# Performance work log

Measured on AMD Instinct MI355X. Metric: run time of the kernel, lower is better.

## Reference

```python
import jax, jax.numpy as jnp
import numpy as np

NUM_EXPERTS = 8
TOP_K = 2
HIDDEN = 2048
INTER = 1024
B, S = 4, 1024


def setup_inputs() -> dict:
    key = jax.random.key(0)
    ks = jax.random.split(key, 5)
    sx = 1.0 / np.sqrt(HIDDEN)
    si = 1.0 / np.sqrt(INTER)
    return {
        "x": jax.random.normal(ks[0], (B, S, HIDDEN), dtype=jnp.float32),
        # router gate: Linear(hidden -> num_experts), weight stored [E, H] (torch convention)
        "gate_w": jax.random.normal(ks[1], (NUM_EXPERTS, HIDDEN), dtype=jnp.float32) * sx,
        # stacked expert weights: gate/up [E, I, H], down [E, H, I]
        "gate_proj_w": jax.random.normal(ks[2], (NUM_EXPERTS, INTER, HIDDEN), dtype=jnp.float32) * sx,
        "up_proj_w": jax.random.normal(ks[3], (NUM_EXPERTS, INTER, HIDDEN), dtype=jnp.float32) * sx,
        "down_proj_w": jax.random.normal(ks[4], (NUM_EXPERTS, HIDDEN, INTER), dtype=jnp.float32) * si,
    }


def _moe_forward(x, gate_w, gate_proj_w, up_proj_w, down_proj_w):
    Bx, Sx, H = x.shape
    T = Bx * Sx
    h = x.reshape(T, H)
    # --- routing (Qwen3: softmax in fp32, top-k, renormalize) ---
    router_logits = h @ gate_w.T                                   # [T, E]
    probs = jax.nn.softmax(router_logits.astype(jnp.float32), axis=-1)
    top_vals, top_idx = jax.lax.top_k(probs, TOP_K)                # [T, K]
    top_vals = top_vals / jnp.sum(top_vals, axis=-1, keepdims=True)  # norm_topk_prob
    # dense routing weights [T, E]: zero for unselected experts
    rw = jnp.zeros((T, NUM_EXPERTS), dtype=jnp.float32)
    rw = rw.at[jnp.arange(T)[:, None], top_idx].add(top_vals)
    rw = rw.astype(h.dtype)
    # --- SwiGLU experts, computed densely and masked by routing weights ---
    g = jnp.einsum('th,eih->tei', h, gate_proj_w)                  # [T, E, I]
    u = jnp.einsum('th,eih->tei', h, up_proj_w)                    # [T, E, I]
    a = jax.nn.silu(g) * u                                         # [T, E, I]
    out_e = jnp.einsum('tei,ehi->teh', a, down_proj_w)             # [T, E, H]
    out = jnp.einsum('te,teh->th', rw, out_e)                      # [T, H]
    return out.reshape(Bx, Sx, H)


def reference(x, gate_w, gate_proj_w, up_proj_w, down_proj_w):
    return _moe_forward(x, gate_w, gate_proj_w, up_proj_w, down_proj_w)
```

## Files before the change

kernel.cpp:

```cpp
#include <hip/hip_runtime.h>
#include <hip/hip_bf16.h>

#define NUM_EXPERTS 8
#define HIDDEN 2048
#define INTER 1024
#define T_TOKENS 4096

#define BK 32
#define GU_BM 64
#define GU_BN 128
#define DN_BM 64
#define DN_BN 128

typedef __attribute__((ext_vector_type(8))) short short8;
typedef __attribute__((ext_vector_type(4))) float f32x4;

__device__ __forceinline__ ushort f2bf(float f) {
    __hip_bfloat16 h = __float2bfloat16(f);
    return *reinterpret_cast<ushort*>(&h);
}

__device__ __forceinline__ void load_lds16(const void* g, void* lds) {
    __builtin_amdgcn_global_load_lds(
        (const __attribute__((address_space(1))) void*)g,
        (__attribute__((address_space(3))) void*)lds, 16, 0, 0);
}

__global__ __launch_bounds__(256) void cvt_bf16(const float* __restrict__ in,
                                                ushort* __restrict__ out, int n4) {
    int i = blockIdx.x * 256 + threadIdx.x;
    int stride = gridDim.x * 256;
    for (; i < n4; i += stride) {
        float4 v = reinterpret_cast<const float4*>(in)[i];
        ushort4 o;
        o.x = f2bf(v.x); o.y = f2bf(v.y); o.z = f2bf(v.z); o.w = f2bf(v.w);
        reinterpret_cast<ushort4*>(out)[i] = o;
    }
}

__global__ __launch_bounds__(64) void moe_router(const float* __restrict__ x,
                                                 const float* __restrict__ gw,
                                                 int* __restrict__ top_idx,
                                                 float* __restrict__ top_w,
                                                 int* __restrict__ counts) {
    int t = blockIdx.x;
    int lane = threadIdx.x;
    const float* xt = x + (size_t)t * HIDDEN;
    float acc[NUM_EXPERTS];
#pragma unroll
    for (int e = 0; e < NUM_EXPERTS; e++) acc[e] = 0.f;
    for (int h = lane; h < HIDDEN; h += 64) {
        float xv = xt[h];
#pragma unroll
        for (int e = 0; e < NUM_EXPERTS; e++)
            acc[e] = fmaf(xv, gw[e * HIDDEN + h], acc[e]);
    }
#pragma unroll
    for (int e = 0; e < NUM_EXPERTS; e++) {
#pragma unroll
        for (int off = 32; off > 0; off >>= 1)
            acc[e] += __shfl_xor(acc[e], off);
    }
    if (lane == 0) {
        int i1 = 0; float l1 = acc[0];
#pragma unroll
        for (int e = 1; e < NUM_EXPERTS; e++)
            if (acc[e] > l1) { l1 = acc[e]; i1 = e; }
        int i2 = -1; float l2 = -3.4e38f;
#pragma unroll
        for (int e = 0; e < NUM_EXPERTS; e++)
            if (e != i1 && acc[e] > l2) { l2 = acc[e]; i2 = e; }
        float w2 = __expf(l2 - l1);
        float denom = 1.f + w2;
        top_idx[t * 2 + 0] = i1;
        top_idx[t * 2 + 1] = i2;
        top_w[t * 2 + 0] = 1.f / denom;
        top_w[t * 2 + 1] = w2 / denom;
        atomicAdd(&counts[i1], 1);
        atomicAdd(&counts[i2], 1);
    }
}

__global__ void moe_offsets(const int* __restrict__ counts,
                            int* __restrict__ ebase, int* __restrict__ cursor) {
    if (threadIdx.x == 0 && blockIdx.x == 0) {
        int s = 0;
        for (int e = 0; e < NUM_EXPERTS; e++) {
            ebase[e] = s; cursor[e] = s; s += counts[e];
        }
    }
}

__global__ __launch_bounds__(256) void moe_scatter(const int* __restrict__ top_idx,
                                                   const float* __restrict__ top_w,
                                                   int* __restrict__ cursor,
                                                   int* __restrict__ slot_tok,
                                                   float* __restrict__ slot_w) {
    int t = blockIdx.x * 256 + threadIdx.x;
    if (t >= T_TOKENS) return;
#pragma unroll
    for (int k = 0; k < 2; k++) {
        int e = top_idx[t * 2 + k];
        int pos = atomicAdd(&cursor[e], 1);
        slot_tok[pos] = t;
        slot_w[pos] = top_w[t * 2 + k];
    }
}

__global__ __launch_bounds__(256, 3) void moe_gateup(const ushort* __restrict__ xb,
                                                     const ushort* __restrict__ wgb,
                                                     const ushort* __restrict__ wub,
                                                     const int* __restrict__ slot_tok,
                                                     const int* __restrict__ ebase,
                                                     const int* __restrict__ ecnt,
                                                     ushort* __restrict__ act) {
    __shared__ ushort ldsA[2][GU_BM * BK];
    __shared__ ushort ldsG[2][GU_BN * BK];
    __shared__ ushort ldsU[2][GU_BN * BK];

    const int e = blockIdx.z;
    const int bm = blockIdx.y;
    const int bn = blockIdx.x;
    const int cnt = ecnt[e];
    if (bm * GU_BM >= cnt) return;
    const int b0 = ebase[e];

    const int tid = threadIdx.x;
    const int lane = tid & 63;
    const int wid = tid >> 6;
    const int wr = wid >> 1, wc = wid & 1;

    const int r = tid >> 2, cs = tid & 3;
    const int scl = (cs ^ ((r >> 1) & 3)) * 8;
    const int ar = bm * GU_BM + r;
    const int tok = slot_tok[b0 + ((ar < cnt) ? ar : (cnt - 1))];
    const ushort* pA = xb + (size_t)tok * HIDDEN + scl;
    const size_t wrow0 = (size_t)e * INTER + (size_t)(bn * GU_BN + r);
    const ushort* pG0 = wgb + wrow0 * HIDDEN + scl;
    const ushort* pG1 = pG0 + (size_t)64 * HIDDEN;
    const ushort* pU0 = wub + wrow0 * HIDDEN + scl;
    const ushort* pU1 = pU0 + (size_t)64 * HIDDEN;

    const int fr = lane & 15;
    const int colsw = (((lane >> 4) ^ ((fr >> 1) & 3)) * 8);

    f32x4 accg[2][4] = {};
    f32x4 accu[2][4] = {};

#define GU_STAGE(buf, t)                                              \
    do {                                                              \
        const int _o = (t) * BK;                                      \
        load_lds16(pA + _o,  &ldsA[buf][tid * 8]);                    \
        load_lds16(pG0 + _o, &ldsG[buf][tid * 8]);                    \
        load_lds16(pG1 + _o, &ldsG[buf][2048 + tid * 8]);             \
        load_lds16(pU0 + _o, &ldsU[buf][tid * 8]);                    \
        load_lds16(pU1 + _o, &ldsU[buf][2048 + tid * 8]);             \
    } while (0)

    GU_STAGE(0, 0);
    __syncthreads();

    int cur = 0;
    const int NT = HIDDEN / BK;
    for (int t = 0; t < NT; ++t) {
        if (t + 1 < NT) GU_STAGE(cur ^ 1, t + 1);

        const ushort* LA = ldsA[cur];
        const ushort* LG = ldsG[cur];
        const ushort* LU = ldsU[cur];
        short8 a[2], bg[4], bu[4];
#pragma unroll
        for (int m = 0; m < 2; m++)
            a[m] = *(const short8*)(LA + (wr * 32 + m * 16 + fr) * BK + colsw);
#pragma unroll
        for (int n = 0; n < 4; n++) {
            bg[n] = *(const short8*)(LG + (wc * 64 + n * 16 + fr) * BK + colsw);
            bu[n] = *(const short8*)(LU + (wc * 64 + n * 16 + fr) * BK + colsw);
        }
#pragma unroll
        for (int m = 0; m < 2; m++) {
#pragma unroll
            for (int n = 0; n < 4; n++) {
                accg[m][n] = __builtin_amdgcn_mfma_f32_16x16x32_bf16(a[m], bg[n], accg[m][n], 0, 0, 0);
                accu[m][n] = __builtin_amdgcn_mfma_f32_16x16x32_bf16(a[m], bu[n], accu[m][n], 0, 0, 0);
            }
        }
        __syncthreads();
        cur ^= 1;
    }
#undef GU_STAGE

#pragma unroll
    for (int m = 0; m < 2; m++) {
#pragma unroll
        for (int rr = 0; rr < 4; rr++) {
            int row = bm * GU_BM + wr * 32 + m * 16 + (lane >> 4) * 4 + rr;
            if (row < cnt) {
                size_t arow = (size_t)(b0 + row) * INTER;
#pragma unroll
                for (int n = 0; n < 4; n++) {
                    int col = bn * GU_BN + wc * 64 + n * 16 + fr;
                    float g = accg[m][n][rr];
                    float u = accu[m][n][rr];
                    float s = g / (1.f + __expf(-g));
                    act[arow + col] = f2bf(s * u);
                }
            }
        }
    }
}

__global__ __launch_bounds__(256, 4) void moe_down(const ushort* __restrict__ act,
                                                   const ushort* __restrict__ wdb,
                                                   const int* __restrict__ slot_tok,
                                                   const float* __restrict__ slot_w,
                                                   const int* __restrict__ ebase,
                                                   const int* __restrict__ ecnt,
                                                   float* __restrict__ out) {
    __shared__ ushort ldsA[2][DN_BM * BK];
    __shared__ ushort ldsB[2][DN_BN * BK];

    const int e = blockIdx.z;
    const int bm = blockIdx.y;
    const int bn = blockIdx.x;
    const int cnt = ecnt[e];
    if (bm * DN_BM >= cnt) return;
    const int b0 = ebase[e];

    const int tid = threadIdx.x;
    const int lane = tid & 63;
    const int wid = tid >> 6;
    const int wr = wid >> 1, wc = wid & 1;

    const int r = tid >> 2, cs = tid & 3;
    const int scl = (cs ^ ((r >> 1) & 3)) * 8;
    const int ar = bm * DN_BM + r;
    const int sr = b0 + ((ar < cnt) ? ar : (cnt - 1));
    const ushort* pA = act + (size_t)sr * INTER + scl;
    const size_t wrow = (size_t)e * HIDDEN + (size_t)(bn * DN_BN + r);
    const ushort* pB0 = wdb + wrow * INTER + scl;
    const ushort* pB1 = pB0 + (size_t)64 * INTER;

    const int fr = lane & 15;
    const int colsw = (((lane >> 4) ^ ((fr >> 1) & 3)) * 8);

    f32x4 acc[2][4] = {};

#define DN_STAGE(buf, t)                                              \
    do {                                                              \
        const int _o = (t) * BK;                                      \
        load_lds16(pA + _o,  &ldsA[buf][tid * 8]);                    \
        load_lds16(pB0 + _o, &ldsB[buf][tid * 8]);                    \
        load_lds16(pB1 + _o, &ldsB[buf][2048 + tid * 8]);             \
    } while (0)

    DN_STAGE(0, 0);
    __syncthreads();

    int cur = 0;
    const int NT = INTER / BK;
    for (int t = 0; t < NT; ++t) {
        if (t + 1 < NT) DN_STAGE(cur ^ 1, t + 1);

        const ushort* LA = ldsA[cur];
        const ushort* LB = ldsB[cur];
        short8 a[2], b[4];
#pragma unroll
        for (int m = 0; m < 2; m++)
            a[m] = *(const short8*)(LA + (wr * 32 + m * 16 + fr) * BK + colsw);
#pragma unroll
        for (int n = 0; n < 4; n++)
            b[n] = *(const short8*)(LB + (wc * 64 + n * 16 + fr) * BK + colsw);
#pragma unroll
        for (int m = 0; m < 2; m++) {
#pragma unroll
            for (int n = 0; n < 4; n++)
                acc[m][n] = __builtin_amdgcn_mfma_f32_16x16x32_bf16(a[m], b[n], acc[m][n], 0, 0, 0);
        }
        __syncthreads();
        cur ^= 1;
    }
#undef DN_STAGE

#pragma unroll
    for (int m = 0; m < 2; m++) {
#pragma unroll
        for (int rr = 0; rr < 4; rr++) {
            int row = bm * DN_BM + wr * 32 + m * 16 + (lane >> 4) * 4 + rr;
            if (row < cnt) {
                int slot = b0 + row;
                int tok = slot_tok[slot];
                float w = slot_w[slot];
                float* orow = out + (size_t)tok * HIDDEN;
#pragma unroll
                for (int n = 0; n < 4; n++) {
                    int col = bn * DN_BN + wc * 64 + n * 16 + fr;
                    atomicAdd(&orow[col], acc[m][n][rr] * w);
                }
            }
        }
    }
}

extern "C" void kernel_launch(void* const* d_in, const int* in_sizes, int n_in,
                              void* d_out, int out_size, void* d_ws, size_t ws_size,
                              hipStream_t stream) {
    const float* x  = (const float*)d_in[0];
    const float* gw = (const float*)d_in[1];
    const float* wg = (const float*)d_in[2];
    const float* wu = (const float*)d_in[3];
    const float* wd = (const float*)d_in[4];
    float* out = (float*)d_out;

    char* ws = (char*)d_ws;
    ushort* xb  = (ushort*)(ws);
    ushort* wgb = (ushort*)(ws + 16777216);
    ushort* wub = (ushort*)(ws + 16777216 + 33554432);
    ushort* wdb = (ushort*)(ws + 16777216 + 2u * 33554432);
    ushort* act = (ushort*)(ws + 16777216 + 3u * 33554432);
    char* p = ws + 2u * 16777216 + 3u * 33554432;
    int*   top_idx  = (int*)p;   p += 32768;
    float* top_w    = (float*)p; p += 32768;
    int*   slot_tok = (int*)p;   p += 32768;
    float* slot_w   = (float*)p; p += 32768;
    int*   counts   = (int*)p;   p += 128;
    int*   ebase    = (int*)p;   p += 128;
    int*   cursor   = (int*)p;   p += 128;

    hipMemsetAsync(counts, 0, 128, stream);
    hipMemsetAsync(d_out, 0, (size_t)out_size * sizeof(float), stream);

    cvt_bf16<<<1024, 256, 0, stream>>>(x,  xb,  (T_TOKENS * HIDDEN) / 4);
    cvt_bf16<<<1024, 256, 0, stream>>>(wg, wgb, (NUM_EXPERTS * INTER * HIDDEN) / 4);
    cvt_bf16<<<1024, 256, 0, stream>>>(wu, wub, (NUM_EXPERTS * INTER * HIDDEN) / 4);
    cvt_bf16<<<1024, 256, 0, stream>>>(wd, wdb, (NUM_EXPERTS * HIDDEN * INTER) / 4);

    moe_router<<<T_TOKENS, 64, 0, stream>>>(x, gw, top_idx, top_w, counts);
    moe_offsets<<<1, 64, 0, stream>>>(counts, ebase, cursor);
    moe_scatter<<<(T_TOKENS + 255) / 256, 256, 0, stream>>>(top_idx, top_w, cursor, slot_tok, slot_w);

    moe_gateup<<<dim3(INTER / GU_BN, T_TOKENS / GU_BM, NUM_EXPERTS), 256, 0, stream>>>(
        xb, wgb, wub, slot_tok, ebase, counts, act);
    moe_down<<<dim3(HIDDEN / DN_BN, T_TOKENS / DN_BM, NUM_EXPERTS), 256, 0, stream>>>(
        act, wdb, slot_tok, slot_w, ebase, counts, out);
}
```

Baseline: 616.9 us.

## Deepen GEMM prefetch with manual waitcnt, remap grid for XCD locality, pack router

Both expert GEMM kernels switch from a double buffer refilled one tile ahead to a scheme that issues loads two tiles ahead. They use explicit s_waitcnt vmcnt/lgkmcnt and s_barrier in place of two __syncthreads per iteration, aiming to overlap global-to-LDS loads with MFMA work. The 3D grids become 1D grids whose block index is remapped so that consecutive blocks on the same XCD handle the same expert, improving L2 reuse of weights. Occupancy hints are raised, and the router packs four tokens per 256-thread block. The hand-placed waitcnt counts depend on exact instruction counts per stage and could race if the compiler reorders or merges loads.

```diff
diff --git a/kernel.cpp b/kernel.cpp
--- a/kernel.cpp
+++ b/kernel.cpp
@@ -38,13 +38,15 @@
     }
 }
 
-__global__ __launch_bounds__(64) void moe_router(const float* __restrict__ x,
-                                                 const float* __restrict__ gw,
-                                                 int* __restrict__ top_idx,
-                                                 float* __restrict__ top_w,
-                                                 int* __restrict__ counts) {
-    int t = blockIdx.x;
-    int lane = threadIdx.x;
+__global__ __launch_bounds__(256) void moe_router(const float* __restrict__ x,
+                                                  const float* __restrict__ gw,
+                                                  int* __restrict__ top_idx,
+                                                  float* __restrict__ top_w,
+                                                  int* __restrict__ counts) {
+    int wid = threadIdx.x >> 6;
+    int lane = threadIdx.x & 63;
+    int t = blockIdx.x * 4 + wid;
+    if (t >= T_TOKENS) return;
     const float* xt = x + (size_t)t * HIDDEN;
     float acc[NUM_EXPERTS];
 #pragma unroll
@@ -107,7 +109,7 @@
     }
 }
 
-__global__ __launch_bounds__(256, 3) void moe_gateup(const ushort* __restrict__ xb,
+__global__ __launch_bounds__(256, 4) void moe_gateup(const ushort* __restrict__ xb,
                                                      const ushort* __restrict__ wgb,
                                                      const ushort* __restrict__ wub,
                                                      const int* __restrict__ slot_tok,
@@ -118,9 +120,13 @@
     __shared__ ushort ldsG[2][GU_BN * BK];
     __shared__ ushort ldsU[2][GU_BN * BK];
 
-    const int e = blockIdx.z;
-    const int bm = blockIdx.y;
-    const int bn = blockIdx.x;
+    const int wg = blockIdx.x;
+    const int wgid = (wg & 7) * 512 + (wg >> 3);
+    const int e = wgid >> 9;
+    const int rem = wgid & 511;
+    const int bm = rem & 63;
+    const int bn = rem >> 6;
+
     const int cnt = ecnt[e];
     if (bm * GU_BM >= cnt) return;
     const int b0 = ebase[e];
@@ -157,37 +163,51 @@
         load_lds16(pU1 + _o, &ldsU[buf][2048 + tid * 8]);             \
     } while (0)
 
+#define GU_FRAGS_MFMA(cur)                                            \
+    do {                                                              \
+        const ushort* LA = ldsA[cur];                                 \
+        const ushort* LG = ldsG[cur];                                 \
+        const ushort* LU = ldsU[cur];                                 \
+        short8 a[2], bg[4], bu[4];                                    \
+        _Pragma("unroll")                                             \
+        for (int m = 0; m < 2; m++)                                   \
+            a[m] = *(const short8*)(LA + (wr * 32 + m * 16 + fr) * BK + colsw); \
+        _Pragma("unroll")                                             \
+        for (int n = 0; n < 4; n++) {                                 \
+            bg[n] = *(const short8*)(LG + (wc * 64 + n * 16 + fr) * BK + colsw); \
+            bu[n] = *(const short8*)(LU + (wc * 64 + n * 16 + fr) * BK + colsw); \
+        }                                                             \
+        asm volatile("s_waitcnt lgkmcnt(0)" ::: "memory");            \
+        asm volatile("s_barrier" ::: "memory");                       \
+        if (t + 2 < NT) GU_STAGE(cur, t + 2);                         \
+        _Pragma("unroll")                                             \
+        for (int m = 0; m < 2; m++) {                                 \
+            _Pragma("unroll")                                         \
+            for (int n = 0; n < 4; n++) {                             \
+                accg[m][n] = __builtin_amdgcn_mfma_f32_16x16x32_bf16(a[m], bg[n], accg[m][n], 0, 0, 0); \
+                accu[m][n] = __builtin_amdgcn_mfma_f32_16x16x32_bf16(a[m], bu[n], accu[m][n], 0, 0, 0); \
+            }                                                         \
+        }                                                             \
+    } while (0)
+
+    const int NT = HIDDEN / BK;
     GU_STAGE(0, 0);
-    __syncthreads();
-
-    int cur = 0;
-    const int NT = HIDDEN / BK;
-    for (int t = 0; t < NT; ++t) {
-        if (t + 1 < NT) GU_STAGE(cur ^ 1, t + 1);
-
-        const ushort* LA = ldsA[cur];
-        const ushort* LG = ldsG[cur];
-        const ushort* LU = ldsU[cur];
-        short8 a[2], bg[4], bu[4];
-#pragma unroll
-        for (int m = 0; m < 2; m++)
-            a[m] = *(const short8*)(LA + (wr * 32 + m * 16 + fr) * BK + colsw);
-#pragma unroll
-        for (int n = 0; n < 4; n++) {
-            bg[n] = *(const short8*)(LG + (wc * 64 + n * 16 + fr) * BK + colsw);
-            bu[n] = *(const short8*)(LU + (wc * 64 + n * 16 + fr) * BK + colsw);
-        }
-#pragma unroll
-        for (int m = 0; m < 2; m++) {
-#pragma unroll
-            for (int n = 0; n < 4; n++) {
-                accg[m][n] = __builtin_amdgcn_mfma_f32_16x16x32_bf16(a[m], bg[n], accg[m][n], 0, 0, 0);
-                accu[m][n] = __builtin_amdgcn_mfma_f32_16x16x32_bf16(a[m], bu[n], accu[m][n], 0, 0, 0);
-            }
-        }
-        __syncthreads();
-        cur ^= 1;
-    }
+    GU_STAGE(1, 1);
+
+    for (int t = 0; t < NT - 1; ++t) {
+        asm volatile("s_waitcnt vmcnt(5)" ::: "memory");
+        asm volatile("s_barrier" ::: "memory");
+        const int cur = t & 1;
+        GU_FRAGS_MFMA(cur);
+    }
+    {
+        const int t = NT - 1;
+        asm volatile("s_waitcnt vmcnt(0)" ::: "memory");
+        asm volatile("s_barrier" ::: "memory");
+        const int cur = t & 1;
+        GU_FRAGS_MFMA(cur);
+    }
+#undef GU_FRAGS_MFMA
 #undef GU_STAGE
 
 #pragma unroll
@@ -210,7 +230,7 @@
     }
 }
 
-__global__ __launch_bounds__(256, 4) void moe_down(const ushort* __restrict__ act,
+__global__ __launch_bounds__(256, 6) void moe_down(const ushort* __restrict__ act,
                                                    const ushort* __restrict__ wdb,
                                                    const int* __restrict__ slot_tok,
                                                    const float* __restrict__ slot_w,
@@ -220,9 +240,13 @@
     __shared__ ushort ldsA[2][DN_BM * BK];
     __shared__ ushort ldsB[2][DN_BN * BK];
 
-    const int e = blockIdx.z;
-    const int bm = blockIdx.y;
-    const int bn = blockIdx.x;
+    const int wg = blockIdx.x;
+    const int wgid = (wg & 7) * 1024 + (wg >> 3);
+    const int e = wgid >> 10;
+    const int rem = wgid & 1023;
+    const int bm = rem & 63;
+    const int bn = rem >> 6;
+
     const int cnt = ecnt[e];
     if (bm * DN_BM >= cnt) return;
     const int b0 = ebase[e];
@@ -254,32 +278,46 @@
         load_lds16(pB1 + _o, &ldsB[buf][2048 + tid * 8]);             \
     } while (0)
 
+#define DN_FRAGS_MFMA(cur)                                            \
+    do {                                                              \
+        const ushort* LA = ldsA[cur];                                 \
+        const ushort* LB = ldsB[cur];                                 \
+        short8 a[2], b[4];                                            \
+        _Pragma("unroll")                                             \
+        for (int m = 0; m < 2; m++)                                   \
+            a[m] = *(const short8*)(LA + (wr * 32 + m * 16 + fr) * BK + colsw); \
+        _Pragma("unroll")                                             \
+        for (int n = 0; n < 4; n++)                                   \
+            b[n] = *(const short8*)(LB + (wc * 64 + n * 16 + fr) * BK + colsw); \
+        asm volatile("s_waitcnt lgkmcnt(0)" ::: "memory");            \
+        asm volatile("s_barrier" ::: "memory");                       \
+        if (t + 2 < NT) DN_STAGE(cur, t + 2);                         \
+        _Pragma("unroll")                                             \
+        for (int m = 0; m < 2; m++) {                                 \
+            _Pragma("unroll")                                         \
+            for (int n = 0; n < 4; n++)                               \
+                acc[m][n] = __builtin_amdgcn_mfma_f32_16x16x32_bf16(a[m], b[n], acc[m][n], 0, 0, 0); \
+        }                                                             \
+    } while (0)
+
+    const int NT = INTER / BK;
     DN_STAGE(0, 0);
-    __syncthreads();
-
-    int cur = 0;
-    const int NT = INTER / BK;
-    for (int t = 0; t < NT; ++t) {
-        if (t + 1 < NT) DN_STAGE(cur ^ 1, t + 1);
-
-        const ushort* LA = ldsA[cur];
-        const ushort* LB = ldsB[cur];
-        short8 a[2], b[4];
-#pragma unroll
-        for (int m = 0; m < 2; m++)
-            a[m] = *(const short8*)(LA + (wr * 32 + m * 16 + fr) * BK + colsw);
-#pragma unroll
-        for (int n = 0; n < 4; n++)
-            b[n] = *(const short8*)(LB + (wc * 64 + n * 16 + fr) * BK + colsw);
-#pragma unroll
-        for (int m = 0; m < 2; m++) {
-#pragma unroll
-            for (int n = 0; n < 4; n++)
-                acc[m][n] = __builtin_amdgcn_mfma_f32_16x16x32_bf16(a[m], b[n], acc[m][n], 0, 0, 0);
-        }
-        __syncthreads();
-        cur ^= 1;
-    }
+    DN_STAGE(1, 1);
+
+    for (int t = 0; t < NT - 1; ++t) {
+        asm volatile("s_waitcnt vmcnt(3)" ::: "memory");
+        asm volatile("s_barrier" ::: "memory");
+        const int cur = t & 1;
+        DN_FRAGS_MFMA(cur);
+    }
+    {
+        const int t = NT - 1;
+        asm volatile("s_waitcnt vmcnt(0)" ::: "memory");
+        asm volatile("s_barrier" ::: "memory");
+        const int cur = t & 1;
+        DN_FRAGS_MFMA(cur);
+    }
+#undef DN_FRAGS_MFMA
 #undef DN_STAGE
 
 #pragma unroll
@@ -335,12 +373,10 @@
     cvt_bf16<<<1024, 256, 0, stream>>>(wu, wub, (NUM_EXPERTS * INTER * HIDDEN) / 4);
     cvt_bf16<<<1024, 256, 0, stream>>>(wd, wdb, (NUM_EXPERTS * HIDDEN * INTER) / 4);
 
-    moe_router<<<T_TOKENS, 64, 0, stream>>>(x, gw, top_idx, top_w, counts);
+    moe_router<<<T_TOKENS / 4, 256, 0, stream>>>(x, gw, top_idx, top_w, counts);
     moe_offsets<<<1, 64, 0, stream>>>(counts, ebase, cursor);
     moe_scatter<<<(T_TOKENS + 255) / 256, 256, 0, stream>>>(top_idx, top_w, cursor, slot_tok, slot_w);
 
-    moe_gateup<<<dim3(INTER / GU_BN, T_TOKENS / GU_BM, NUM_EXPERTS), 256, 0, stream>>>(
-        xb, wgb, wub, slot_tok, ebase, counts, act);
-    moe_down<<<dim3(HIDDEN / DN_BN, T_TOKENS / DN_BM, NUM_EXPERTS), 256, 0, stream>>>(
-        act, wdb, slot_tok, slot_w, ebase, counts, out);
-}
+    moe_gateup<<<4096, 256, 0, stream>>>(xb, wgb, wub, slot_tok, ebase, counts, act);
+    moe_down<<<8192, 256, 0, stream>>>(act, wdb, slot_tok, slot_w, ebase, counts, out);
+}
```

Result: no change. 617.4 us (+0.1%).
